# Performance work log

Measured on AMD Instinct MI355X. Metric: run time of the kernel, lower is better.

## Reference

```python
import jax, jax.numpy as jnp
import numpy as np

MASK_P = 0.15
MASK_LEN = 8
B, H, W, C = 64, 512, 256, 4


def setup_inputs() -> dict:
    key = jax.random.key(0)
    k1, k2, k3, k4, k5 = jax.random.split(key, 5)
    x = jax.random.normal(k1, (B, H, W, C), dtype=jnp.float32)
    time_rand = jax.random.uniform(k2, (B, MASK_LEN, W, C), dtype=jnp.float32)
    freq_rand = jax.random.uniform(k3, (B, H, MASK_LEN, C), dtype=jnp.float32)
    time_starts = jax.random.randint(k4, (B,), 0, H - MASK_LEN + 1, dtype=jnp.int32)
    freq_starts = jax.random.randint(k5, (B,), 0, W - MASK_LEN + 1, dtype=jnp.int32)
    return {"x": x, "time_rand": time_rand, "freq_rand": freq_rand,
            "time_starts": time_starts, "freq_starts": freq_starts}


def _combined_mask(time_rand, freq_rand, time_starts, freq_starts, h, w):
    # Bernoulli masks from uniform draws (cast of comparison, like tf.cast(u < p))
    tmask = jnp.where(time_rand < MASK_P, 1.0, 0.0)   # [B, L, W, C]
    fmask = jnp.where(freq_rand < MASK_P, 1.0, 0.0)   # [B, H, L, C]

    # --- time masking: pad each sample's [L,W,C] strip to height h at start_i,
    # then (faithful to the original broadcast) take product over the batch.
    rel_h = jnp.arange(h)[None, :] - time_starts[:, None]          # [B, H]
    valid_h = (rel_h >= 0) & (rel_h < MASK_LEN)                    # [B, H]
    idx_h = jnp.clip(rel_h, 0, MASK_LEN - 1)[:, :, None, None]    # [B, H, 1, 1]
    padded_t = jnp.take_along_axis(tmask, idx_h, axis=1)           # [B, H, W, C]
    padded_t = jnp.where(valid_h[:, :, None, None], padded_t, 0.0)
    mask_t = jnp.prod(1.0 - padded_t, axis=0)                      # [H, W, C]

    # --- freq masking, same pattern along the width axis.
    rel_w = jnp.arange(w)[None, :] - freq_starts[:, None]          # [B, W]
    valid_w = (rel_w >= 0) & (rel_w < MASK_LEN)                    # [B, W]
    idx_w = jnp.clip(rel_w, 0, MASK_LEN - 1)[:, None, :, None]    # [B, 1, W, 1]
    padded_f = jnp.take_along_axis(fmask, idx_w, axis=2)           # [B, H, W, C]
    padded_f = jnp.where(valid_w[:, None, :, None], padded_f, 0.0)
    mask_f = jnp.prod(1.0 - padded_f, axis=0)                      # [H, W, C]

    return mask_t * mask_f                                         # [H, W, C]


def reference(x, time_rand, freq_rand, time_starts, freq_starts):
    b, h, w, c = x.shape
    mask = _combined_mask(time_rand, freq_rand, time_starts, freq_starts, h, w)
    return x * mask[None]  # same mask broadcast over batch, as in the original
```

## Files before the change

### kernel.cpp

```cpp
#include <hip/hip_runtime.h>

constexpr int B_ = 64, H_ = 512, W_ = 256, C_ = 4, L_ = 8;
constexpr int WC    = W_ * C_;
constexpr int HWC   = H_ * WC;
constexpr int MWC4  = HWC / 4;
constexpr long long N4 = 8388608LL;

__global__ __launch_bounds__(256)
void build_mask(const float* __restrict__ trand, const float* __restrict__ frand,
                const int* __restrict__ tstart, const int* __restrict__ fstart,
                float* __restrict__ mask) {
    __shared__ int ts_s[B_], fs_s[B_];
    const int t = threadIdx.x;
    const int h = blockIdx.x;
    if (t < B_) { ts_s[t] = tstart[t]; fs_s[t] = fstart[t]; }
    __syncthreads();

    float m0 = 1.f, m1 = 1.f, m2 = 1.f, m3 = 1.f;
    for (int b = 0; b < B_; ++b) {
        int lt = h - ts_s[b];
        if ((unsigned)lt < (unsigned)L_) {
            float4 v = *(const float4*)(trand + ((b * L_ + lt) * W_ + t) * C_);
            if (v.x < 0.15f) m0 = 0.f;
            if (v.y < 0.15f) m1 = 0.f;
            if (v.z < 0.15f) m2 = 0.f;
            if (v.w < 0.15f) m3 = 0.f;
        }
        int lw = t - fs_s[b];
        if ((unsigned)lw < (unsigned)L_) {
            float4 v = *(const float4*)(frand + ((b * H_ + h) * L_ + lw) * C_);
            if (v.x < 0.15f) m0 = 0.f;
            if (v.y < 0.15f) m1 = 0.f;
            if (v.z < 0.15f) m2 = 0.f;
            if (v.w < 0.15f) m3 = 0.f;
        }
    }
    *(float4*)(mask + (h * W_ + t) * C_) = make_float4(m0, m1, m2, m3);
}

__global__ __launch_bounds__(256)
void apply_mask(const float4* __restrict__ x4, const float4* __restrict__ m4,
                float4* __restrict__ out4) {
    const int base = blockIdx.x * 1024 + threadIdx.x;
    float4 a0 = x4[base];
    float4 a1 = x4[base + 256];
    float4 a2 = x4[base + 512];
    float4 a3 = x4[base + 768];
    float4 b0 = m4[ base         & (MWC4 - 1)];
    float4 b1 = m4[(base +  256) & (MWC4 - 1)];
    float4 b2 = m4[(base +  512) & (MWC4 - 1)];
    float4 b3 = m4[(base +  768) & (MWC4 - 1)];
    a0.x *= b0.x; a0.y *= b0.y; a0.z *= b0.z; a0.w *= b0.w;
    a1.x *= b1.x; a1.y *= b1.y; a1.z *= b1.z; a1.w *= b1.w;
    a2.x *= b2.x; a2.y *= b2.y; a2.z *= b2.z; a2.w *= b2.w;
    a3.x *= b3.x; a3.y *= b3.y; a3.z *= b3.z; a3.w *= b3.w;
    out4[base]       = a0;
    out4[base + 256] = a1;
    out4[base + 512] = a2;
    out4[base + 768] = a3;
}

constexpr int ROWS = 2, BCH = 8;
__global__ __launch_bounds__(256)
void mask_apply_fused(const float* __restrict__ x, const float* __restrict__ trand,
                      const float* __restrict__ frand, const int* __restrict__ tstart,
                      const int* __restrict__ fstart, float* __restrict__ out) {
    __shared__ int flagw[ROWS * WC / 4];
    __shared__ int ts_s[B_], fs_s[B_];
    unsigned char* flags = (unsigned char*)flagw;
    const int t = threadIdx.x, h0 = blockIdx.x * ROWS, b0 = blockIdx.y * BCH;
    flagw[2 * t] = 0; flagw[2 * t + 1] = 0;
    if (t < B_) { ts_s[t] = tstart[t]; fs_s[t] = fstart[t]; }
    __syncthreads();
    for (int b = 0; b < B_; ++b) {
        int ts = ts_s[b];
#pragma unroll
        for (int r = 0; r < ROWS; ++r) {
            int l = h0 + r - ts;
            if ((unsigned)l < (unsigned)L_) {
                const float* row = trand + (b * L_ + l) * WC;
#pragma unroll
                for (int k = 0; k < 4; ++k)
                    if (row[t * 4 + k] < 0.15f) flags[r * WC + t * 4 + k] = 1;
            }
        }
    }
    {
        int bsub = t >> 5, lane = t & 31, l = lane >> 2, c = lane & 3;
        for (int bb = 0; bb < B_; bb += 8) {
            int b = bb + bsub, fs = fs_s[b];
#pragma unroll
            for (int r = 0; r < ROWS; ++r) {
                float vf = frand[(b * H_ + h0 + r) * (L_ * C_) + l * C_ + c];
                if (vf < 0.15f) flags[r * WC + (fs + l) * C_ + c] = 1;
            }
        }
    }
    __syncthreads();
    const unsigned fw0 = (unsigned)flagw[t], fw1 = (unsigned)flagw[256 + t];
    for (int bi = 0; bi < BCH; ++bi) {
        int base = (b0 + bi) * HWC + h0 * WC;
        float4 v0 = ((const float4*)(x + base))[t];
        float4 v1 = ((const float4*)(x + base + WC))[t];
        if (fw0 & 0xffu)       v0.x = 0.f;
        if (fw0 & 0xff00u)     v0.y = 0.f;
        if (fw0 & 0xff0000u)   v0.z = 0.f;
        if (fw0 & 0xff000000u) v0.w = 0.f;
        if (fw1 & 0xffu)       v1.x = 0.f;
        if (fw1 & 0xff00u)     v1.y = 0.f;
        if (fw1 & 0xff0000u)   v1.z = 0.f;
        if (fw1 & 0xff000000u) v1.w = 0.f;
        ((float4*)(out + base))[t]      = v0;
        ((float4*)(out + base + WC))[t] = v1;
    }
}

extern "C" void kernel_launch(void* const* d_in, const int* in_sizes, int n_in,
                              void* d_out, int out_size, void* d_ws, size_t ws_size,
                              hipStream_t stream) {
    const float* x  = (const float*)d_in[0];
    const float* tr = (const float*)d_in[1];
    const float* fr = (const float*)d_in[2];
    const int*   ts = (const int*)d_in[3];
    const int*   fs = (const int*)d_in[4];
    float* out = (float*)d_out;

    if (ws_size >= (size_t)HWC * sizeof(float)) {
        float* mask = (float*)d_ws;
        build_mask<<<H_, 256, 0, stream>>>(tr, fr, ts, fs, mask);
        apply_mask<<<(int)(N4 / 1024), 256, 0, stream>>>(
            (const float4*)x, (const float4*)mask, (float4*)out);
    } else {
        dim3 grid(H_ / ROWS, B_ / BCH);
        mask_apply_fused<<<grid, 256, 0, stream>>>(x, tr, fr, ts, fs, out);
    }
}
```

Measured before the change: 251.6 us.

## Scatter byte flags for mask, apply via packed flags and nontemporal stores

Replaces the per-row gather mask builder with a memset plus a scatter kernel that reads each random draw once and writes byte flags at the target positions. The apply kernel now reads packed 8-bit flags, a quarter of the bytes of the float mask, zeroes lanes by testing bits, and writes the output with nontemporal stores. This cuts mask traffic and the scan over all batches per row, at the cost of an extra memset launch and racy but idempotent byte writes.

```diff
diff --git a/kernel.cpp b/kernel.cpp
--- a/kernel.cpp
+++ b/kernel.cpp
@@ -1,63 +1,66 @@
 #include <hip/hip_runtime.h>
 
 constexpr int B_ = 64, H_ = 512, W_ = 256, C_ = 4, L_ = 8;
-constexpr int WC    = W_ * C_;
-constexpr int HWC   = H_ * WC;
-constexpr int MWC4  = HWC / 4;
+constexpr int WC     = W_ * C_;
+constexpr int HWC    = H_ * WC;
+constexpr int HWC4   = HWC / 4;
+constexpr int N_TIME = B_ * L_ * WC;
+constexpr int N_FREQ = B_ * H_ * L_ * C_;
 constexpr long long N4 = 8388608LL;
 
+typedef float floatx4 __attribute__((ext_vector_type(4)));
+
 __global__ __launch_bounds__(256)
-void build_mask(const float* __restrict__ trand, const float* __restrict__ frand,
-                const int* __restrict__ tstart, const int* __restrict__ fstart,
-                float* __restrict__ mask) {
-    __shared__ int ts_s[B_], fs_s[B_];
-    const int t = threadIdx.x;
-    const int h = blockIdx.x;
-    if (t < B_) { ts_s[t] = tstart[t]; fs_s[t] = fstart[t]; }
-    __syncthreads();
-
-    float m0 = 1.f, m1 = 1.f, m2 = 1.f, m3 = 1.f;
-    for (int b = 0; b < B_; ++b) {
-        int lt = h - ts_s[b];
-        if ((unsigned)lt < (unsigned)L_) {
-            float4 v = *(const float4*)(trand + ((b * L_ + lt) * W_ + t) * C_);
-            if (v.x < 0.15f) m0 = 0.f;
-            if (v.y < 0.15f) m1 = 0.f;
-            if (v.z < 0.15f) m2 = 0.f;
-            if (v.w < 0.15f) m3 = 0.f;
+void scatter_mask(const float* __restrict__ trand, const float* __restrict__ frand,
+                  const int* __restrict__ tstart, const int* __restrict__ fstart,
+                  unsigned char* __restrict__ flags) {
+    int tid = blockIdx.x * 256 + threadIdx.x;
+    if (tid < N_TIME) {
+        if (trand[tid] < 0.15f) {
+            int wc = tid & (WC - 1);
+            int l  = (tid >> 10) & (L_ - 1);
+            int b  = tid >> 13;
+            int h  = tstart[b] + l;
+            flags[h * WC + wc] = 1;
         }
-        int lw = t - fs_s[b];
-        if ((unsigned)lw < (unsigned)L_) {
-            float4 v = *(const float4*)(frand + ((b * H_ + h) * L_ + lw) * C_);
-            if (v.x < 0.15f) m0 = 0.f;
-            if (v.y < 0.15f) m1 = 0.f;
-            if (v.z < 0.15f) m2 = 0.f;
-            if (v.w < 0.15f) m3 = 0.f;
+    } else {
+        int j = tid - N_TIME;
+        if (frand[j] < 0.15f) {
+            int c = j & (C_ - 1);
+            int l = (j >> 2) & (L_ - 1);
+            int h = (j >> 5) & (H_ - 1);
+            int b = j >> 14;
+            int w = fstart[b] + l;
+            flags[h * WC + w * C_ + c] = 1;
         }
     }
-    *(float4*)(mask + (h * W_ + t) * C_) = make_float4(m0, m1, m2, m3);
 }
 
 __global__ __launch_bounds__(256)
-void apply_mask(const float4* __restrict__ x4, const float4* __restrict__ m4,
-                float4* __restrict__ out4) {
+void apply_mask(const floatx4* __restrict__ x4,
+                const unsigned int* __restrict__ flag32,
+                floatx4* __restrict__ out4) {
     const int base = blockIdx.x * 1024 + threadIdx.x;
-    float4 a0 = x4[base];
-    float4 a1 = x4[base + 256];
-    float4 a2 = x4[base + 512];
-    float4 a3 = x4[base + 768];
-    float4 b0 = m4[ base         & (MWC4 - 1)];
-    float4 b1 = m4[(base +  256) & (MWC4 - 1)];
-    float4 b2 = m4[(base +  512) & (MWC4 - 1)];
-    float4 b3 = m4[(base +  768) & (MWC4 - 1)];
-    a0.x *= b0.x; a0.y *= b0.y; a0.z *= b0.z; a0.w *= b0.w;
-    a1.x *= b1.x; a1.y *= b1.y; a1.z *= b1.z; a1.w *= b1.w;
-    a2.x *= b2.x; a2.y *= b2.y; a2.z *= b2.z; a2.w *= b2.w;
-    a3.x *= b3.x; a3.y *= b3.y; a3.z *= b3.z; a3.w *= b3.w;
-    out4[base]       = a0;
-    out4[base + 256] = a1;
-    out4[base + 512] = a2;
-    out4[base + 768] = a3;
+    floatx4 a0 = x4[base];
+    floatx4 a1 = x4[base + 256];
+    floatx4 a2 = x4[base + 512];
+    floatx4 a3 = x4[base + 768];
+    unsigned f0 = flag32[ base         & (HWC4 - 1)];
+    unsigned f1 = flag32[(base +  256) & (HWC4 - 1)];
+    unsigned f2 = flag32[(base +  512) & (HWC4 - 1)];
+    unsigned f3 = flag32[(base +  768) & (HWC4 - 1)];
+    if (f0 & 0xffu) a0.x = 0.f;  if (f0 & 0xff00u) a0.y = 0.f;
+    if (f0 & 0xff0000u) a0.z = 0.f;  if (f0 & 0xff000000u) a0.w = 0.f;
+    if (f1 & 0xffu) a1.x = 0.f;  if (f1 & 0xff00u) a1.y = 0.f;
+    if (f1 & 0xff0000u) a1.z = 0.f;  if (f1 & 0xff000000u) a1.w = 0.f;
+    if (f2 & 0xffu) a2.x = 0.f;  if (f2 & 0xff00u) a2.y = 0.f;
+    if (f2 & 0xff0000u) a2.z = 0.f;  if (f2 & 0xff000000u) a2.w = 0.f;
+    if (f3 & 0xffu) a3.x = 0.f;  if (f3 & 0xff00u) a3.y = 0.f;
+    if (f3 & 0xff0000u) a3.z = 0.f;  if (f3 & 0xff000000u) a3.w = 0.f;
+    __builtin_nontemporal_store(a0, &out4[base]);
+    __builtin_nontemporal_store(a1, &out4[base + 256]);
+    __builtin_nontemporal_store(a2, &out4[base + 512]);
+    __builtin_nontemporal_store(a3, &out4[base + 768]);
 }
 
 constexpr int ROWS = 2, BCH = 8;
@@ -125,11 +128,12 @@
     const int*   fs = (const int*)d_in[4];
     float* out = (float*)d_out;
 
-    if (ws_size >= (size_t)HWC * sizeof(float)) {
-        float* mask = (float*)d_ws;
-        build_mask<<<H_, 256, 0, stream>>>(tr, fr, ts, fs, mask);
+    if (ws_size >= (size_t)HWC) {
+        unsigned char* flags = (unsigned char*)d_ws;
+        (void)hipMemsetAsync(flags, 0, HWC, stream);
+        scatter_mask<<<(N_TIME + N_FREQ) / 256, 256, 0, stream>>>(tr, fr, ts, fs, flags);
         apply_mask<<<(int)(N4 / 1024), 256, 0, stream>>>(
-            (const float4*)x, (const float4*)mask, (float4*)out);
+            (const floatx4*)x, (const unsigned int*)flags, (floatx4*)out);
     } else {
         dim3 grid(H_ / ROWS, B_ / BCH);
         mask_apply_fused<<<grid, 256, 0, stream>>>(x, tr, fr, ts, fs, out);
```

Result: faster. 245.5 us (-2.4%).
